# Optimization experiments

Hardware: AMD Instinct MI355X
Metric: run time of the kernel (lower is better)

The kernel has to match this reference:

```python
import jax, jax.numpy as jnp
import numpy as np

D_MODEL = 1024
D_INNER = 2048
D_STATE = 16
D_CONV = 4
DT_RANK = 64  # ceil(D_MODEL / 16)
BATCH = 2
SEQLEN = 2048


def setup_inputs() -> dict:
    key = jax.random.key(0)
    ks = jax.random.split(key, 9)
    s = 0.02
    hidden_states = jax.random.normal(ks[0], (BATCH, SEQLEN, D_MODEL), dtype=jnp.float32)
    W_in = jax.random.normal(ks[1], (D_MODEL, 2 * D_INNER), dtype=jnp.float32) * s
    # flax depthwise Conv kernel layout: (window, in_features//groups=1, out_features)
    conv_kernel = jax.random.normal(ks[2], (D_CONV, 1, D_INNER), dtype=jnp.float32) * 0.2
    conv_bias = jax.random.normal(ks[3], (D_INNER,), dtype=jnp.float32) * s
    W_x = jax.random.normal(ks[4], (D_INNER, DT_RANK + 2 * D_STATE), dtype=jnp.float32) * s
    W_dt = jax.random.normal(ks[5], (DT_RANK, D_INNER), dtype=jnp.float32) * s
    b_dt = jax.random.normal(ks[6], (D_INNER,), dtype=jnp.float32) * s
    # A_log = log(arange(1, d_state+1)) broadcast over d_inner (constant init in module)
    A_log = jnp.log(jnp.broadcast_to(jnp.arange(1, D_STATE + 1, dtype=jnp.float32), (D_INNER, D_STATE)))
    D = jnp.ones((D_INNER,), dtype=jnp.float32)
    W_out = jax.random.normal(ks[7], (D_INNER, D_MODEL), dtype=jnp.float32) * s
    return {
        "hidden_states": hidden_states,
        "W_in": W_in,
        "conv_kernel": conv_kernel,
        "conv_bias": conv_bias,
        "W_x": W_x,
        "W_dt": W_dt,
        "b_dt": b_dt,
        "A_log": A_log,
        "D": D,
        "W_out": W_out,
    }


def _mamba_forward(hidden_states, W_in, conv_kernel, conv_bias, W_x, W_dt, b_dt, A_log, D, W_out):
    # in_proj, then einops '(d i)' split with i=2 => interleaved channels
    xz = hidden_states @ W_in                       # (b, l, 2*d_inner)
    x = xz[..., 0::2]                               # (b, l, d_inner)
    z = xz[..., 1::2]                               # (b, l, d_inner)

    # depthwise conv1d, padding='SAME' (as in flax nn.Conv)
    x = jax.lax.conv_general_dilated(
        x, conv_kernel, window_strides=(1,), padding="SAME",
        dimension_numbers=("NWC", "WIO", "NWC"),
        feature_group_count=D_INNER,
    ) + conv_bias
    x = jax.nn.silu(x)

    x_dbl = x @ W_x                                 # (b, l, dt_rank + 2*d_state)
    dt = x_dbl[..., :DT_RANK] @ W_dt + b_dt         # (b, l, d_inner)
    Bm = x_dbl[..., DT_RANK:DT_RANK + D_STATE]      # (b, l, n)
    Cm = x_dbl[..., DT_RANK + D_STATE:]             # (b, l, n)

    A = -jnp.exp(A_log.astype(jnp.float32))         # (d_inner, n)
    delta = jax.nn.softplus(dt.astype(jnp.float32)) # (b, l, d_inner)

    deltaA = jnp.exp(jnp.einsum("bld,dn->lbdn", delta, A))          # (l, b, d, n)
    deltaB_u = jnp.einsum("bld,bln,bld->lbdn", delta, Bm, x)        # (l, b, d, n)
    C_l = jnp.transpose(Cm, (1, 0, 2))                               # (l, b, n)

    state0 = jnp.zeros((BATCH, D_INNER, D_STATE), dtype=jnp.float32)

    def step(state, inputs):
        dA, dBu, c = inputs
        state = dA * state + dBu                    # (b, d, n)
        y = jnp.einsum("bdn,bn->bd", state, c)      # (b, d)
        return state, y

    _, y = jax.lax.scan(step, state0, (deltaA, deltaB_u, C_l))
    y = jnp.transpose(y, (1, 0, 2))                 # (b, l, d_inner)

    out = (y + x * D) * jax.nn.silu(z)              # skip via D, gate via silu(z)
    return out @ W_out                              # (b, l, d_model)


def reference(hidden_states, W_in, conv_kernel, conv_bias, W_x, W_dt, b_dt, A_log, D, W_out):
    return _mamba_forward(hidden_states, W_in, conv_kernel, conv_bias, W_x, W_dt, b_dt, A_log, D, W_out)
```

## Files before the change

kernel.cpp:

```cpp
#include <hip/hip_runtime.h>
#include <hip/hip_bf16.h>

typedef unsigned short u16;
typedef __attribute__((ext_vector_type(8))) short short8;
typedef __attribute__((ext_vector_type(4))) short short4v;
typedef __attribute__((ext_vector_type(4))) float f32x4;
typedef __attribute__((ext_vector_type(4))) float float4v;
typedef __attribute__((ext_vector_type(2))) float f32x2;

#define DMODEL 1024
#define DI 2048
#define NST 16
#define RANK 64
#define BB 2
#define LL 2048
#define MM (BB*LL)
#define LC 64
#define NCH (LL/LC)

__device__ __forceinline__ float b2f(u16 v){ union{unsigned u; float f;}x; x.u=(unsigned)v<<16; return x.f; }
__device__ __forceinline__ u16 f2b(float f){
  union{unsigned u; float f;}x; x.f=f;
  unsigned r = x.u + 0x7FFFu + ((x.u>>16)&1u);
  return (u16)(r>>16);
}
__device__ __forceinline__ bool probe_bf(const u16* probe){ return probe[1] != 0; }
__device__ __forceinline__ float ldin(const void* p, size_t i, bool bf){
  return bf ? b2f(((const u16*)p)[i]) : ((const float*)p)[i];
}
__device__ __forceinline__ u16 ldb(const void* p, size_t i, bool bf){
  return bf ? ((const u16*)p)[i] : f2b(((const float*)p)[i]);
}
__device__ __forceinline__ void gl16(const u16* g, char* lds_wave_base){
  __builtin_amdgcn_global_load_lds((const __attribute__((address_space(1))) unsigned*)g,
                                   (__attribute__((address_space(3))) unsigned*)lds_wave_base, 16, 0, 0);
}

template<int EPI>
__global__ __launch_bounds__(256,2) void mgemm_k(
    const u16* __restrict__ A, const u16* __restrict__ Bt,
    void* __restrict__ O0, void* __restrict__ O1,
    const void* __restrict__ bias, const u16* __restrict__ probe,
    int M, int N, int K, int lda, int ldb, int ldc)
{
  const bool bf = probe_bf(probe);
  __shared__ char smem[(EPI==3||EPI==4) ? 33792 : 16384];
  const int t = threadIdx.x;
  int bx = blockIdx.x, by = blockIdx.y;
  {
    const int gx = gridDim.x;
    const int nwg = gx*gridDim.y;
    const int lin = by*gx + bx;
    const int swz = (lin & 7)*(nwg>>3) + (lin>>3);
    bx = swz % gx; by = swz / gx;
  }
  const int m0 = by*128, n0 = bx*128;
  const int kbeg = blockIdx.z * K;
  const int lane = t & 63;
  const int wv = t >> 6;
  const int wm = (wv>>1)*64, wn = (wv&1)*64;
  const int lr = lane & 15, q = lane >> 4;

  const int r0 = t>>2, q0 = t&3;
  const u16* Ag0 = A + kbeg + (size_t)(m0 + r0)*lda + q0*8;
  const u16* Ag1 = A + kbeg + (size_t)(m0 + 64 + r0)*lda + q0*8;
  const u16* Bg0 = Bt + kbeg + (size_t)(n0 + r0)*ldb + q0*8;
  const u16* Bg1 = Bt + kbeg + (size_t)(n0 + 64 + r0)*ldb + q0*8;
  char* const wbase = smem + (t & ~63)*16;
  char* const lA0 = wbase;
  char* const lA1 = wbase + 4096;
  char* const lB0 = wbase + 8192;
  char* const lB1 = wbase + 12288;

  int aro[4], bro[4];
#pragma unroll
  for(int i=0;i<4;i++) aro[i] = (wm + i*16 + lr)*64 + q*16;
#pragma unroll
  for(int j=0;j<4;j++) bro[j] = (wn + j*16 + lr)*64 + q*16;

  f32x4 acc[4][4];
#pragma unroll
  for(int i=0;i<4;i++)
#pragma unroll
    for(int j=0;j<4;j++) acc[i][j] = (f32x4){0.f,0.f,0.f,0.f};

  for(int k0=0;k0<K;k0+=32){
    __syncthreads();
    gl16(Ag0 + k0, lA0); gl16(Ag1 + k0, lA1);
    gl16(Bg0 + k0, lB0); gl16(Bg1 + k0, lB1);
    __syncthreads();
    short8 af[4], bfv[4];
#pragma unroll
    for(int i=0;i<4;i++) af[i] = *(const short8*)(smem + aro[i]);
#pragma unroll
    for(int j=0;j<4;j++) bfv[j] = *(const short8*)(smem + 8192 + bro[j]);
#pragma unroll
    for(int i=0;i<4;i++)
#pragma unroll
      for(int j=0;j<4;j++)
        acc[i][j] = __builtin_amdgcn_mfma_f32_16x16x32_bf16(af[i], bfv[j], acc[i][j], 0,0,0);
  }

  if(EPI==3 || EPI==4){
    float bj[4];
    if(EPI==3){
#pragma unroll
      for(int j=0;j<4;j++) bj[j] = ldin(bias, n0 + wn + j*16 + lr, bf);
    }
    __syncthreads();
    u16* tile = (u16*)smem;
#pragma unroll
    for(int i=0;i<4;i++)
#pragma unroll
      for(int r=0;r<4;r++){
        int trow = wm + i*16 + q*4 + r;
#pragma unroll
        for(int j=0;j<4;j++){
          int tcol = wn + j*16 + lr;
          float v = acc[i][j][r];
          if(EPI==3){
            float s = v + bj[j];
            v = (s > 20.f) ? s : log1pf(__expf(s));
          }
          tile[trow*132 + tcol] = f2b(v);
        }
      }
    __syncthreads();
    u16* obase;
    int cb;
    if(EPI==4){ obase = (n0 < DI) ? (u16*)O0 : (u16*)O1; cb = n0 & (DI-1); }
    else      { obase = (u16*)O0; cb = n0; }
    const int oc = (EPI==4) ? DI : ldc;
#pragma unroll
    for(int it=0;it<8;it++){
      int idx = it*256 + t;
      int row = idx >> 4;
      int colc = (idx & 15) * 8;
      short8 v = *(const short8*)(tile + row*132 + colc);
      *(short8*)(obase + (size_t)(m0+row)*oc + cb + colc) = v;
    }
    return;
  }
#pragma unroll
  for(int i=0;i<4;i++){
#pragma unroll
    for(int r=0;r<4;r++){
      int row = m0 + wm + i*16 + q*4 + r;
#pragma unroll
      for(int j=0;j<4;j++){
        int col = n0 + wn + j*16 + lr;
        float v = acc[i][j][r];
        if(EPI==1){
          ((float*)O0)[(size_t)blockIdx.z*M*ldc + (size_t)row*ldc + col] = v;
        } else {
          if(bf) ((u16*)O0)[(size_t)row*ldc + col] = f2b(v);
          else   ((float*)O0)[(size_t)row*ldc + col] = v;
        }
      }
    }
  }
}

__device__ __forceinline__ void tr_block(
    const void* src, u16* dst, int R, int C, int bx, int by, bool bf, bool perm,
    int tid, u16 (*tile)[33])
{
  const int c0 = bx*32, r0 = by*32;
  const int tc = tid & 31, tr0 = tid >> 5;
#pragma unroll
  for(int i=0;i<4;i++){
    int r = tr0 + i*8;
    int gc = c0 + tc;
    tile[r][tc] = (gc < C) ? ldb(src, (size_t)(r0+r)*C + gc, bf) : (u16)0;
  }
  __syncthreads();
#pragma unroll
  for(int i=0;i<4;i++){
    int dr = c0 + tr0 + i*8;
    if(perm) dr = (dr>>1) + ((dr&1)<<11);
    int dc = r0 + tc;
    dst[(size_t)dr*R + dc] = tile[tc][tr0 + i*8];
  }
}

__global__ __launch_bounds__(256) void prep_k(
    const void* __restrict__ W_in, const void* __restrict__ W_out,
    const void* __restrict__ W_x, const void* __restrict__ W_dt,
    const void* __restrict__ hidden,
    u16* __restrict__ WinT, u16* __restrict__ WoutT, u16* __restrict__ WxT,
    u16* __restrict__ WdtT, u16* __restrict__ hb, const u16* __restrict__ probe)
{
  const bool bf = probe_bf(probe);
  __shared__ u16 tile[32][33];
  const int bid = blockIdx.x, t = threadIdx.x;
  if(bid < 4096){
    tr_block(W_in, WinT, DMODEL, 2*DI, bid & 127, bid >> 7, bf, true, t, tile);
  } else if(bid < 6144){
    int b2 = bid - 4096; tr_block(W_out, WoutT, DI, DMODEL, b2 & 31, b2 >> 5, bf, false, t, tile);
  } else if(bid < 6400){
    int b2 = bid - 6144; tr_block(W_x, WxT, DI, 96, b2 & 3, b2 >> 2, bf, false, t, tile);
  } else if(bid < 6528){
    int b2 = bid - 6400; tr_block(W_dt, WdtT, RANK, DI, b2 & 63, b2 >> 6, bf, false, t, tile);
  } else {
    size_t i = ((size_t)(bid - 6528)*256 + t)*8;
    if(bf){
      *(short8*)(hb+i) = *(const short8*)((const u16*)hidden + i);
    } else {
      float4v a = *(const float4v*)((const float*)hidden + i);
      float4v b = *(const float4v*)((const float*)hidden + i + 4);
      short8 r;
      r[0]=(short)f2b(a[0]); r[1]=(short)f2b(a[1]); r[2]=(short)f2b(a[2]); r[3]=(short)f2b(a[3]);
      r[4]=(short)f2b(b[0]); r[5]=(short)f2b(b[1]); r[6]=(short)f2b(b[2]); r[7]=(short)f2b(b[3]);
      *(short8*)(hb+i) = r;
    }
  }
}

__global__ __launch_bounds__(256) void redx_k(
    const float* __restrict__ P, float* __restrict__ xdbl, u16* __restrict__ xdblb)
{
  size_t i = ((size_t)blockIdx.x*256 + threadIdx.x)*4;
  float4v s = *(const float4v*)(P + i);
#pragma unroll
  for(int p=1;p<8;p++) s += *(const float4v*)(P + (size_t)p*MM*128 + i);
  *(float4v*)(xdbl + i) = s;
  short4v r; r[0]=(short)f2b(s[0]); r[1]=(short)f2b(s[1]); r[2]=(short)f2b(s[2]); r[3]=(short)f2b(s[3]);
  *(short4v*)(xdblb + i) = r;
}

__global__ __launch_bounds__(256) void red7_k(
    const float* __restrict__ P, void* __restrict__ out, const u16* __restrict__ probe)
{
  const bool bf = probe_bf(probe);
  size_t i = ((size_t)blockIdx.x*256 + threadIdx.x)*4;
  float4v a = *(const float4v*)(P + i);
  float4v b = *(const float4v*)(P + (size_t)MM*DMODEL + i);
  float4v s = a + b;
  if(bf){
    short4v r; r[0]=(short)f2b(s[0]); r[1]=(short)f2b(s[1]); r[2]=(short)f2b(s[2]); r[3]=(short)f2b(s[3]);
    *(short4v*)((u16*)out + i) = r;
  } else {
    *(float4v*)((float*)out + i) = s;
  }
}

__global__ __launch_bounds__(256) void conv_silu_k(
  const u16* __restrict__ xb, const void* __restrict__ w,
  const void* __restrict__ bias, u16* __restrict__ xcb,
  const u16* __restrict__ probe)
{
  const bool bf = probe_bf(probe);
  const int row = blockIdx.x;
  const int tt = row & (LL-1);
  const int d = threadIdx.x*8;
  float wv[4][8], bv[8];
  if(bf){
    short8 bb = *(const short8*)((const u16*)bias + d);
#pragma unroll
    for(int j=0;j<8;j++) bv[j] = b2f((u16)bb[j]);
#pragma unroll
    for(int k=0;k<4;k++){
      short8 ww = *(const short8*)((const u16*)w + k*DI + d);
#pragma unroll
      for(int j=0;j<8;j++) wv[k][j] = b2f((u16)ww[j]);
    }
  } else {
    *(float4v*)(bv)   = *(const float4v*)((const float*)bias + d);
    *(float4v*)(bv+4) = *(const float4v*)((const float*)bias + d + 4);
#pragma unroll
    for(int k=0;k<4;k++){
      *(float4v*)(wv[k])   = *(const float4v*)((const float*)w + k*DI + d);
      *(float4v*)(wv[k]+4) = *(const float4v*)((const float*)w + k*DI + d + 4);
    }
  }
  float acc[8];
#pragma unroll
  for(int j=0;j<8;j++) acc[j] = bv[j];
  const u16* xrow = xb + (size_t)row*DI + d;
#pragma unroll
  for(int k=0;k<4;k++){
    int o = tt - 1 + k;
    if(0<=o && o<LL){
      short8 xv = *(const short8*)(xrow + (ptrdiff_t)(k-1)*DI);
#pragma unroll
      for(int j=0;j<8;j++) acc[j] = fmaf(b2f((u16)xv[j]), wv[k][j], acc[j]);
    }
  }
  short8 sb;
#pragma unroll
  for(int j=0;j<8;j++){ float s = acc[j] / (1.f + __expf(-acc[j])); sb[j]=(short)f2b(s); }
  *(short8*)(xcb + (size_t)row*DI + d) = sb;
}

__global__ __launch_bounds__(256) void scan_a_k(
  const u16* __restrict__ dlb, const u16* __restrict__ xcb,
  const float* __restrict__ xdbl, const void* __restrict__ A_log,
  float* __restrict__ Bacc, float* __restrict__ sumdv,
  const u16* __restrict__ probe)
{
  const bool bf = probe_bf(probe);
  __shared__ float Bsh[LC][NST];
  const int t = threadIdx.x;
  const int d0 = blockIdx.x*512 + 2*t;
  const int b = blockIdx.y, c = blockIdx.z;
  for(int i=t;i<LC*NST;i+=256){
    int l = i>>4, n = i&15;
    Bsh[l][n] = xdbl[((size_t)b*LL + (size_t)c*LC + l)*128 + 64 + n];
  }
  __syncthreads();
  float ac[2][NST], s[2][NST];
#pragma unroll
  for(int ch=0;ch<2;ch++)
#pragma unroll
    for(int n=0;n<NST;n++){
      ac[ch][n] = -__expf(ldin(A_log, (size_t)(d0+ch)*NST+n, bf));
      s[ch][n]=0.f;
    }
  bool geom = true;
#pragma unroll
  for(int ch=0;ch<2;ch++){
    float a0 = ac[ch][0];
#pragma unroll
    for(int n=1;n<NST;n++) geom = geom && (fabsf(ac[ch][n]-(n+1)*a0) <= 1e-4f*(n+1)*fabsf(a0));
  }
  float sum0=0.f, sum1=0.f;
  const size_t base0 = ((size_t)b*LL + (size_t)c*LC)*DI + d0;
  for(int l=0;l<LC;l++){
    unsigned dp = *(const unsigned*)(dlb + base0 + (size_t)l*DI);
    unsigned xp = *(const unsigned*)(xcb + base0 + (size_t)l*DI);
    float dv0=b2f((u16)(dp&0xffff)), dv1=b2f((u16)(dp>>16));
    float xv0=b2f((u16)(xp&0xffff)), xv1=b2f((u16)(xp>>16));
    float du0=dv0*xv0, du1=dv1*xv1;
    sum0+=dv0; sum1+=dv1;
    if(geom){
      float e0=__expf(ac[0][0]*dv0), e1=__expf(ac[1][0]*dv1);
      float p0=1.f, p1=1.f;
#pragma unroll
      for(int n=0;n<NST;n++){
        float Bv=Bsh[l][n];
        p0*=e0; s[0][n]=fmaf(p0, s[0][n], du0*Bv);
        p1*=e1; s[1][n]=fmaf(p1, s[1][n], du1*Bv);
      }
    } else {
#pragma unroll
      for(int n=0;n<NST;n++){
        float Bv=Bsh[l][n];
        s[0][n]=fmaf(__expf(ac[0][n]*dv0), s[0][n], du0*Bv);
        s[1][n]=fmaf(__expf(ac[1][n]*dv1), s[1][n], du1*Bv);
      }
    }
  }
  const size_t ob = ((size_t)c*BB + b)*((size_t)NST*DI) + d0;
#pragma unroll
  for(int n=0;n<NST;n++){
    f32x2 bs; bs[0]=s[0][n]; bs[1]=s[1][n];
    *(f32x2*)(Bacc + ob + (size_t)n*DI) = bs;
  }
  f32x2 sd; sd[0]=sum0; sd[1]=sum1;
  *(f32x2*)(sumdv + ((size_t)c*BB + b)*DI + d0) = sd;
}

__global__ __launch_bounds__(256) void scan_b_k(
  const float* __restrict__ Bacc, const float* __restrict__ sumdv,
  const void* __restrict__ A_log, float* __restrict__ Sin,
  const u16* __restrict__ probe)
{
  const bool bf = probe_bf(probe);
  const int idx = blockIdx.x*256 + threadIdx.x;
  const int d = idx & (DI-1);
  const int n = (idx >> 11) & 15;
  const int b = idx >> 15;
  const float ac = -__expf(ldin(A_log, (size_t)d*NST+n, bf));
  float s = 0.f;
  for(int c=0;c<NCH;c++){
    size_t off = (size_t)c*((size_t)BB*NST*DI) + idx;
    float a = __expf(ac * sumdv[((size_t)c*BB + b)*DI + d]);
    float bb = Bacc[off];
    Sin[off] = s;
    s = fmaf(a, s, bb);
  }
}

__global__ __launch_bounds__(256) void scan_c_gate_k(
  const u16* __restrict__ dlb, const u16* __restrict__ xcb,
  const float* __restrict__ xdbl, const void* __restrict__ A_log,
  const float* __restrict__ Sin, const u16* __restrict__ zb,
  const void* __restrict__ Dw, u16* __restrict__ G,
  const u16* __restrict__ probe)
{
  const bool bf = probe_bf(probe);
  __shared__ float Bsh[LC][NST], Csh[LC][NST];
  const int t = threadIdx.x;
  const int d0 = blockIdx.x*512 + 2*t;
  const int b = blockIdx.y, c = blockIdx.z;
  for(int i=t;i<LC*NST;i+=256){
    int l = i>>4, n = i&15;
    size_t ro = ((size_t)b*LL + (size_t)c*LC + l)*128;
    Bsh[l][n] = xdbl[ro + 64 + n];
    Csh[l][n] = xdbl[ro + 80 + n];
  }
  __syncthreads();
  float ac[2][NST], s[2][NST];
  const size_t ib = ((size_t)c*BB + b)*((size_t)NST*DI) + d0;
#pragma unroll
  for(int ch=0;ch<2;ch++)
#pragma unroll
    for(int n=0;n<NST;n++)
      ac[ch][n] = -__expf(ldin(A_log, (size_t)(d0+ch)*NST+n, bf));
#pragma unroll
  for(int n=0;n<NST;n++){
    f32x2 si = *(const f32x2*)(Sin + ib + (size_t)n*DI);
    s[0][n]=si[0]; s[1][n]=si[1];
  }
  bool geom = true;
#pragma unroll
  for(int ch=0;ch<2;ch++){
    float a0 = ac[ch][0];
#pragma unroll
    for(int n=1;n<NST;n++) geom = geom && (fabsf(ac[ch][n]-(n+1)*a0) <= 1e-4f*(n+1)*fabsf(a0));
  }
  const float D0 = ldin(Dw, d0, bf), D1 = ldin(Dw, d0+1, bf);
  const size_t base0 = ((size_t)b*LL + (size_t)c*LC)*DI + d0;
  for(int l=0;l<LC;l++){
    const size_t idx = base0 + (size_t)l*DI;
    unsigned dp = *(const unsigned*)(dlb + idx);
    unsigned xp = *(const unsigned*)(xcb + idx);
    unsigned zz = *(const unsigned*)(zb + idx);
    float dv0=b2f((u16)(dp&0xffff)), dv1=b2f((u16)(dp>>16));
    float xv0=b2f((u16)(xp&0xffff)), xv1=b2f((u16)(xp>>16));
    float du0=dv0*xv0, du1=dv1*xv1;
    float y0=0.f, y1=0.f;
    if(geom){
      float e0=__expf(ac[0][0]*dv0), e1=__expf(ac[1][0]*dv1);
      float p0=1.f, p1=1.f;
#pragma unroll
      for(int n=0;n<NST;n++){
        float Bv=Bsh[l][n], Cv=Csh[l][n];
        p0*=e0; s[0][n]=fmaf(p0, s[0][n], du0*Bv); y0=fmaf(s[0][n], Cv, y0);
        p1*=e1; s[1][n]=fmaf(p1, s[1][n], du1*Bv); y1=fmaf(s[1][n], Cv, y1);
      }
    } else {
#pragma unroll
      for(int n=0;n<NST;n++){
        float Bv=Bsh[l][n], Cv=Csh[l][n];
        s[0][n]=fmaf(__expf(ac[0][n]*dv0), s[0][n], du0*Bv); y0=fmaf(s[0][n], Cv, y0);
        s[1][n]=fmaf(__expf(ac[1][n]*dv1), s[1][n], du1*Bv); y1=fmaf(s[1][n], Cv, y1);
      }
    }
    float z0 = b2f((u16)(zz & 0xffff)), z1 = b2f((u16)(zz >> 16));
    float g0 = z0 / (1.f + __expf(-z0));
    float g1 = z1 / (1.f + __expf(-z1));
    float o0 = (y0 + xv0*D0) * g0;
    float o1 = (y1 + xv1*D1) * g1;
    *(unsigned*)(G + idx) = (unsigned)f2b(o0) | ((unsigned)f2b(o1) << 16);
  }
}

extern "C" void kernel_launch(void* const* d_in, const int* in_sizes, int n_in,
                              void* d_out, int out_size, void* d_ws, size_t ws_size,
                              hipStream_t stream)
{
  const void* hidden = d_in[0];
  const void* W_in   = d_in[1];
  const void* convw  = d_in[2];
  const void* convb  = d_in[3];
  const void* W_x    = d_in[4];
  const void* W_dt   = d_in[5];
  const void* b_dt   = d_in[6];
  const u16*  A_log  = (const u16*)d_in[7];
  const void* Dw     = d_in[8];
  const void* W_out  = d_in[9];

  char* p = (char*)d_ws;
  u16*   xb   = (u16*)  p;
  float* Sin  = (float*)p;
  u16*   zb   = (u16*)  (p + 16777216);
  u16*   xcb  = (u16*)  (p + 33554432);
  float* Bcc  = (float*)(p + 67108864);
  u16*   G    = (u16*)  (p + 83886080);
  float* Pw   = (float*)(p + 100663296);
  u16*   dlb  = (u16*)  (p + 100663296);
  float* Pw7  = (float*)(p + 100663296);
  u16*   hb   = (u16*)  (p + 117440512);
  float* sumdv= (float*)(p + 117440512);
  float* xdbl = (float*)(p + 134217728);
  u16*   xdblb= (u16*)  (p + 136314880);
  u16*   WinT = (u16*)  (p + 137363456);
  u16*   WoutT= (u16*)  (p + 145752064);
  u16*   WxT  = (u16*)  (p + 149946368);
  u16*   WdtT = (u16*)  (p + 150470656);

  prep_k<<<6528 + (MM*DMODEL)/(256*8), 256, 0, stream>>>(
      W_in, W_out, W_x, W_dt, hidden, WinT, WoutT, WxT, WdtT, hb, A_log);
  mgemm_k<4><<<dim3(32,32), 256, 0, stream>>>(hb, WinT, xb, zb, nullptr, A_log,
                                              MM, 2*DI, DMODEL, DMODEL, DMODEL, DI);
  conv_silu_k<<<MM, 256, 0, stream>>>(xb, convw, convb, xcb, A_log);
  mgemm_k<1><<<dim3(1,32,8), 256, 0, stream>>>(xcb, WxT, Pw, nullptr, nullptr, A_log,
                                               MM, 128, DI/8, DI, DI, 128);
  redx_k<<<(MM*128)/(256*4), 256, 0, stream>>>(Pw, xdbl, xdblb);
  mgemm_k<3><<<dim3(16,32), 256, 0, stream>>>(xdblb, WdtT, dlb, nullptr, b_dt, A_log,
                                              MM, DI, RANK, 128, RANK, DI);
  scan_a_k<<<dim3(DI/512, BB, NCH), 256, 0, stream>>>(dlb, xcb, xdbl, A_log, Bcc, sumdv, A_log);
  scan_b_k<<<(BB*NST*DI)/256, 256, 0, stream>>>(Bcc, sumdv, A_log, Sin, A_log);
  scan_c_gate_k<<<dim3(DI/512, BB, NCH), 256, 0, stream>>>(dlb, xcb, xdbl, A_log, Sin, zb, Dw, G, A_log);
  mgemm_k<1><<<dim3(DMODEL/128, MM/128, 2), 256, 0, stream>>>(G, WoutT, Pw7, nullptr, nullptr, A_log,
                                                              MM, DMODEL, DI/2, DI, DI, DMODEL);
  red7_k<<<(MM*DMODEL)/(256*4), 256, 0, stream>>>(Pw7, d_out, A_log);
}
```

Measured before the change: 348.9 us.

## Halve scan chunk length and software-prefetch sequential loads in scan kernels

Shrinks the chunk length of the chunked selective scan from 64 to 32, which doubles the number of chunks and gives the chunk-local kernels twice as many blocks for parallelism. In exchange the serial cross-chunk pass gets longer and writes twice as much intermediate state. It also adds register double-buffering, so the delta, x and z loads for steps l+2 and l+3 are issued before computing steps l and l+1, with the next chunk's values prefetched in the cross-chunk kernel. The prefetching is meant to hide global load latency in the sequential recurrence loops.

```diff
diff --git a/kernel.cpp b/kernel.cpp
--- a/kernel.cpp
+++ b/kernel.cpp
@@ -15,7 +15,7 @@
 #define BB 2
 #define LL 2048
 #define MM (BB*LL)
-#define LC 64
+#define LC 32
 #define NCH (LL/LC)
 
 __device__ __forceinline__ float b2f(u16 v){ union{unsigned u; float f;}x; x.u=(unsigned)v<<16; return x.f; }
@@ -325,9 +325,10 @@
   }
   float sum0=0.f, sum1=0.f;
   const size_t base0 = ((size_t)b*LL + (size_t)c*LC)*DI + d0;
-  for(int l=0;l<LC;l++){
-    unsigned dp = *(const unsigned*)(dlb + base0 + (size_t)l*DI);
-    unsigned xp = *(const unsigned*)(xcb + base0 + (size_t)l*DI);
+  const u16* dptr = dlb + base0;
+  const u16* xptr = xcb + base0;
+
+  auto stepA = [&](int l, unsigned dp, unsigned xp){
     float dv0=b2f((u16)(dp&0xffff)), dv1=b2f((u16)(dp>>16));
     float xv0=b2f((u16)(xp&0xffff)), xv1=b2f((u16)(xp>>16));
     float du0=dv0*xv0, du1=dv1*xv1;
@@ -349,7 +350,24 @@
         s[1][n]=fmaf(__expf(ac[1][n]*dv1), s[1][n], du1*Bv);
       }
     }
-  }
+  };
+
+  unsigned dpA = *(const unsigned*)(dptr);
+  unsigned xpA = *(const unsigned*)(xptr);
+  unsigned dpB = *(const unsigned*)(dptr + DI);
+  unsigned xpB = *(const unsigned*)(xptr + DI);
+  for(int l=0;l<LC;l+=2){
+    int l2 = (l+2 < LC) ? l+2 : LC-1;
+    int l3 = (l+3 < LC) ? l+3 : LC-1;
+    unsigned dpC = *(const unsigned*)(dptr + (size_t)l2*DI);
+    unsigned xpC = *(const unsigned*)(xptr + (size_t)l2*DI);
+    unsigned dpD = *(const unsigned*)(dptr + (size_t)l3*DI);
+    unsigned xpD = *(const unsigned*)(xptr + (size_t)l3*DI);
+    stepA(l,   dpA, xpA);
+    stepA(l+1, dpB, xpB);
+    dpA=dpC; xpA=xpC; dpB=dpD; xpB=xpD;
+  }
+
   const size_t ob = ((size_t)c*BB + b)*((size_t)NST*DI) + d0;
 #pragma unroll
   for(int n=0;n<NST;n++){
@@ -372,12 +390,16 @@
   const int b = idx >> 15;
   const float ac = -__expf(ldin(A_log, (size_t)d*NST+n, bf));
   float s = 0.f;
+  float svN = sumdv[((size_t)0*BB + b)*DI + d];
+  float bbN = Bacc[idx];
   for(int c=0;c<NCH;c++){
-    size_t off = (size_t)c*((size_t)BB*NST*DI) + idx;
-    float a = __expf(ac * sumdv[((size_t)c*BB + b)*DI + d]);
-    float bb = Bacc[off];
-    Sin[off] = s;
-    s = fmaf(a, s, bb);
+    int c1 = (c+1 < NCH) ? c+1 : NCH-1;
+    float svC = sumdv[((size_t)c1*BB + b)*DI + d];
+    float bbC = Bacc[(size_t)c1*((size_t)BB*NST*DI) + idx];
+    float a = __expf(ac * svN);
+    Sin[(size_t)c*((size_t)BB*NST*DI) + idx] = s;
+    s = fmaf(a, s, bbN);
+    svN = svC; bbN = bbC;
   }
 }
 
@@ -421,11 +443,11 @@
   }
   const float D0 = ldin(Dw, d0, bf), D1 = ldin(Dw, d0+1, bf);
   const size_t base0 = ((size_t)b*LL + (size_t)c*LC)*DI + d0;
-  for(int l=0;l<LC;l++){
-    const size_t idx = base0 + (size_t)l*DI;
-    unsigned dp = *(const unsigned*)(dlb + idx);
-    unsigned xp = *(const unsigned*)(xcb + idx);
-    unsigned zz = *(const unsigned*)(zb + idx);
+  const u16* dptr = dlb + base0;
+  const u16* xptr = xcb + base0;
+  const u16* zptr = zb  + base0;
+
+  auto stepC = [&](int l, unsigned dp, unsigned xp, unsigned zz){
     float dv0=b2f((u16)(dp&0xffff)), dv1=b2f((u16)(dp>>16));
     float xv0=b2f((u16)(xp&0xffff)), xv1=b2f((u16)(xp>>16));
     float du0=dv0*xv0, du1=dv1*xv1;
@@ -452,7 +474,27 @@
     float g1 = z1 / (1.f + __expf(-z1));
     float o0 = (y0 + xv0*D0) * g0;
     float o1 = (y1 + xv1*D1) * g1;
-    *(unsigned*)(G + idx) = (unsigned)f2b(o0) | ((unsigned)f2b(o1) << 16);
+    *(unsigned*)(G + base0 + (size_t)l*DI) = (unsigned)f2b(o0) | ((unsigned)f2b(o1) << 16);
+  };
+
+  unsigned dpA = *(const unsigned*)(dptr);
+  unsigned xpA = *(const unsigned*)(xptr);
+  unsigned zzA = *(const unsigned*)(zptr);
+  unsigned dpB = *(const unsigned*)(dptr + DI);
+  unsigned xpB = *(const unsigned*)(xptr + DI);
+  unsigned zzB = *(const unsigned*)(zptr + DI);
+  for(int l=0;l<LC;l+=2){
+    int l2 = (l+2 < LC) ? l+2 : LC-1;
+    int l3 = (l+3 < LC) ? l+3 : LC-1;
+    unsigned dpC = *(const unsigned*)(dptr + (size_t)l2*DI);
+    unsigned xpC = *(const unsigned*)(xptr + (size_t)l2*DI);
+    unsigned zzC = *(const unsigned*)(zptr + (size_t)l2*DI);
+    unsigned dpD = *(const unsigned*)(dptr + (size_t)l3*DI);
+    unsigned xpD = *(const unsigned*)(xptr + (size_t)l3*DI);
+    unsigned zzD = *(const unsigned*)(zptr + (size_t)l3*DI);
+    stepC(l,   dpA, xpA, zzA);
+    stepC(l+1, dpB, xpB, zzB);
+    dpA=dpC; xpA=xpC; zzA=zzC; dpB=dpD; xpB=xpD; zzB=zzD;
   }
 }
 
```

Result: faster. 321.6 us (-7.8%).
